# Optimization experiments

Measured on AMD Instinct MI355X. Metric: run time of the kernel, lower is better.

The kernel has to match this reference:

```python
import jax, jax.numpy as jnp
import numpy as np

B, C, H, W = 16, 192, 48, 48
EPS = 1e-5  # torch LayerNorm default


def setup_inputs() -> dict:
    key = jax.random.key(0)
    ks = jax.random.split(key, 5)
    dim = C
    x = jax.random.normal(ks[0], (B, C, H, W), dtype=jnp.float32)
    ln_w = jnp.ones((dim,), dtype=jnp.float32)
    ln_b = jnp.zeros((dim,), dtype=jnp.float32)
    s = 1.0 / np.sqrt(dim)
    Wq = jax.random.uniform(ks[1], (dim, dim), jnp.float32, -s, s)
    Wk = jax.random.uniform(ks[2], (dim, dim), jnp.float32, -s, s)
    Wv = jax.random.uniform(ks[3], (dim, dim), jnp.float32, -s, s)
    w1 = jnp.ones((1,), dtype=jnp.float32)
    w2 = jnp.ones((1,), dtype=jnp.float32)
    return {"x": x, "ln_w": ln_w, "ln_b": ln_b, "Wq": Wq, "Wk": Wk, "Wv": Wv, "w1": w1, "w2": w2}


def reference(x, ln_w, ln_b, Wq, Wk, Wv, w1, w2):
    b, c, h, w = x.shape
    # [B, C, H, W] -> [B, N, C]
    xf = x.reshape(b, c, h * w).transpose(0, 2, 1)
    # LayerNorm over channel dim
    mu = jnp.mean(xf, axis=-1, keepdims=True)
    var = jnp.mean(jnp.square(xf - mu), axis=-1, keepdims=True)
    xn = (xf - mu) * jax.lax.rsqrt(var + EPS) * ln_w + ln_b
    # torch Linear: y = x @ W^T
    Q = jnp.einsum('bnc,dc->bnd', xn, Wq)
    K = jnp.einsum('bnc,dc->bnd', xn, Wk)
    V = jnp.einsum('bnc,dc->bnd', xn, Wv)
    S = jnp.einsum('bnd,bmd->bnm', Q, K)  # [B, N, N]
    attn1 = jax.nn.softmax(S, axis=-1)
    attn2 = jnp.square(jax.nn.relu(S))
    # learned blend weights (softmax over two scalars)
    e1, e2 = jnp.exp(w1), jnp.exp(w2)
    denom = e1 + e2
    attn = (e1 / denom) * attn1 + (e2 / denom) * attn2
    out = jnp.einsum('bnm,bmd->bnd', attn, V)  # [B, N, C]
    out = out.transpose(0, 2, 1).reshape(b, c, h, w)
    return out + x
```

## Files before the change

### kernel.cpp

```cpp
#include <hip/hip_runtime.h>

#define NN 2304
#define CC 192
#define NBATCH 16

typedef unsigned short u16;
typedef __bf16 bf16x8 __attribute__((ext_vector_type(8)));
typedef float f32x4 __attribute__((ext_vector_type(4)));
typedef float f32x16 __attribute__((ext_vector_type(16)));

__device__ __forceinline__ u16 bf16bits(float f) {
  union { float f; unsigned u; } v;
  v.f = f;
  unsigned r = v.u + 0x7FFFu + ((v.u >> 16) & 1u);
  return (u16)(r >> 16);
}

__device__ __forceinline__ uint32_t cvtpk(float lo, float hi) {
  uint32_t d;
  asm("v_cvt_pk_bf16_f32 %0, %1, %2" : "=v"(d) : "v"(lo), "v"(hi));
  return d;
}

__device__ __forceinline__ int swzK(int row, int col) {
  int ch = col >> 3;
  int phys = (ch & ~7) | ((ch ^ row) & 7);
  return row * 192 + (phys << 3) + (col & 7);
}
__device__ __forceinline__ int swz64(int row, int col) {
  int ch = (col >> 3) ^ row;
  return (row << 6) | ((ch & 7) << 3) | (col & 7);
}

__device__ __forceinline__ void gll16(const u16* g, u16* l) {
  __builtin_amdgcn_global_load_lds(
      (const __attribute__((address_space(1))) u16*)g,
      (__attribute__((address_space(3))) u16*)l, 16, 0, 0);
}

__global__ __launch_bounds__(256) void ln_kernel(
    const float* __restrict__ x, const float* __restrict__ lnw,
    const float* __restrict__ lnb, u16* __restrict__ xn) {
  __shared__ float xt[192 * 65];
  __shared__ float psum[4][64], psq[4][64];
  __shared__ float mu_s[64], rs_s[64];
  __shared__ float lw_s[192], lb_s[192];
  int t = threadIdx.x;
  int b = blockIdx.y, n0 = blockIdx.x * 64;
  const float* xb = x + (size_t)b * CC * NN;
  if (t < 192) { lw_s[t] = lnw[t]; lb_s[t] = lnb[t]; }
#pragma unroll
  for (int i = 0; i < 48; ++i) {
    int idx = i * 256 + t;
    int c = idx >> 6, n = idx & 63;
    xt[c * 65 + n] = xb[(size_t)c * NN + n0 + n];
  }
  __syncthreads();
  {
    int n = t & 63, part = t >> 6;
    float s = 0.f, s2 = 0.f;
#pragma unroll
    for (int c = part * 48; c < part * 48 + 48; ++c) {
      float v = xt[c * 65 + n];
      s += v; s2 += v * v;
    }
    psum[part][n] = s; psq[part][n] = s2;
  }
  __syncthreads();
  if (t < 64) {
    float s = psum[0][t] + psum[1][t] + psum[2][t] + psum[3][t];
    float s2 = psq[0][t] + psq[1][t] + psq[2][t] + psq[3][t];
    float mu = s * (1.0f / 192.0f);
    float var = s2 * (1.0f / 192.0f) - mu * mu;
    mu_s[t] = mu;
    rs_s[t] = rsqrtf(var + 1e-5f);
  }
  __syncthreads();
#pragma unroll
  for (int i = 0; i < 12; ++i) {
    int u = i * 256 + t;
    int n = u / 48, cq = (u % 48) * 4;
    float mu = mu_s[n], rs = rs_s[n];
    float v0 = (xt[(cq + 0) * 65 + n] - mu) * rs * lw_s[cq + 0] + lb_s[cq + 0];
    float v1 = (xt[(cq + 1) * 65 + n] - mu) * rs * lw_s[cq + 1] + lb_s[cq + 1];
    float v2 = (xt[(cq + 2) * 65 + n] - mu) * rs * lw_s[cq + 2] + lb_s[cq + 2];
    float v3 = (xt[(cq + 3) * 65 + n] - mu) * rs * lw_s[cq + 3] + lb_s[cq + 3];
    uint2 o;
    o.x = cvtpk(v0, v1);
    o.y = cvtpk(v2, v3);
    *(uint2*)&xn[((size_t)(b * NN + n0 + n)) * CC + cq] = o;
  }
}

__global__ __launch_bounds__(256, 3) void qkv_gemm(
    const u16* __restrict__ xn, const float* __restrict__ Wq,
    const float* __restrict__ Wk, const float* __restrict__ Wv,
    u16* __restrict__ qb, u16* __restrict__ kb, u16* __restrict__ vtb) {
  __shared__ u16 xs[12288];
  __shared__ u16 wsm[12288];
  int t = threadIdx.x, w = t >> 6, lane = t & 63, l15 = lane & 15, qd = lane >> 4;
  int m0 = blockIdx.x * 64, n0 = blockIdx.y * 64, z = blockIdx.z;
  const float* W = (z == 0) ? Wq : (z == 1 ? Wk : Wv);
#pragma unroll
  for (int i = 0; i < 6; ++i) {
    int ch = i * 256 + t;
    int row = ch / 24, cin = (ch % 24) * 8;
    *(uint4*)&xs[swzK(row, cin)] = *(const uint4*)&xn[(size_t)(m0 + row) * 192 + cin];
  }
#pragma unroll
  for (int i = 0; i < 6; ++i) {
    int ch = i * 256 + t;
    int row = ch / 24, cin = (ch % 24) * 8;
    const float* src = &W[(size_t)(n0 + row) * 192 + cin];
    float4 f0 = *(const float4*)src;
    float4 f1 = *(const float4*)(src + 4);
    uint4 o;
    o.x = cvtpk(f0.x, f0.y);
    o.y = cvtpk(f0.z, f0.w);
    o.z = cvtpk(f1.x, f1.y);
    o.w = cvtpk(f1.z, f1.w);
    *(uint4*)&wsm[swzK(row, cin)] = o;
  }
  __syncthreads();
  bf16x8 a[6];
#pragma unroll
  for (int kk = 0; kk < 6; ++kk)
    a[kk] = *(const bf16x8*)&xs[swzK(w * 16 + l15, kk * 32 + qd * 8)];
  const f32x4 fz = {0.f, 0.f, 0.f, 0.f};
  f32x4 acc[4];
#pragma unroll
  for (int ct = 0; ct < 4; ++ct) {
    acc[ct] = fz;
#pragma unroll
    for (int kk = 0; kk < 6; ++kk) {
      bf16x8 bfr = *(const bf16x8*)&wsm[swzK(ct * 16 + l15, kk * 32 + qd * 8)];
      acc[ct] = __builtin_amdgcn_mfma_f32_16x16x32_bf16(a[kk], bfr, acc[ct], 0, 0, 0);
    }
  }
  if (z < 2) {
    u16* outp = (z == 0) ? qb : kb;
#pragma unroll
    for (int ct = 0; ct < 4; ++ct)
#pragma unroll
      for (int r = 0; r < 4; ++r) {
        int m = m0 + w * 16 + qd * 4 + r;
        outp[(size_t)m * 192 + n0 + ct * 16 + l15] = bf16bits(acc[ct][r]);
      }
  } else {
    __syncthreads();
#pragma unroll
    for (int ct = 0; ct < 4; ++ct)
#pragma unroll
      for (int r = 0; r < 4; ++r)
        xs[swz64(ct * 16 + l15, w * 16 + qd * 4 + r)] = bf16bits(acc[ct][r]);
    __syncthreads();
    int b = blockIdx.x / 36, nb = (blockIdx.x % 36) * 64;
#pragma unroll
    for (int i = 0; i < 16; ++i) {
      int idx = i * 256 + t;
      int d = idx >> 6, nn = idx & 63;
      vtb[(size_t)b * 192 * NN + (size_t)(n0 + d) * NN + nb + nn] = xs[swz64(d, nn)];
    }
  }
}

__global__ __launch_bounds__(256, 2) void attn_fused(
    const u16* __restrict__ qb, const u16* __restrict__ kb,
    const u16* __restrict__ vtb, const float* __restrict__ w1p,
    const float* __restrict__ w2p, const float* __restrict__ x,
    float* __restrict__ out) {
  __shared__ u16 sm[32768];
  float* olds = (float*)sm;
  float* lred = (float*)(sm + 24576);

  int t = threadIdx.x, w = t >> 6, lane = t & 63;
  int l31 = lane & 31, hi = lane >> 5;
  int qh = w >> 1, ch = w & 1;
  int bid = blockIdx.x;
  int xcd = bid & 7, j = bid >> 3;
  int b = xcd * 2 + (j >= 36 ? 1 : 0);
  int qt = (j >= 36) ? j - 36 : j;

  const u16* Kg = kb + (size_t)b * NN * CC;
  const u16* Vg = vtb + (size_t)b * CC * NN;
  const u16* Qr = qb + ((size_t)b * NN + qt * 64 + qh * 32 + l31) * CC + hi * 8;
  bf16x8 qf[12];
#pragma unroll
  for (int ks = 0; ks < 12; ++ks) qf[ks] = *(const bf16x8*)(Qr + ks * 16);

  float e1 = __expf(w1p[0]), e2 = __expf(w2p[0]);
  float den = e1 + e2;
  float c1f = e1 / den, c2f = e2 / den;

  u16* pexSW = sm + 24576 + (qh * 2 + ch) * 1024 + lane * 8;
  const u16* pexSR = sm + 24576 + (qh * 2 + (1 - ch)) * 1024 + lane * 8;
  u16* pexRW = sm + 28672 + (qh * 2 + ch) * 1024 + lane * 8;
  const u16* pexRR = sm + 28672 + (qh * 2 + (1 - ch)) * 1024 + lane * 8;

  f32x16 z16;
#pragma unroll
  for (int i = 0; i < 16; ++i) z16[i] = 0.f;
  f32x16 os[3], orl[3];
#pragma unroll
  for (int i = 0; i < 3; ++i) { os[i] = z16; orl[i] = z16; }
  float lsum = 0.f;

#define STAGE_K(KT)                                                        \
  {                                                                        \
    _Pragma("unroll") for (int i = 0; i < 6; ++i) {                        \
      int cid = i * 4 + w, sc = cid * 64 + lane;                           \
      int row = sc / 24, pc = sc % 24;                                     \
      int gc = (pc & ~7) | ((pc ^ row) & 7);                               \
      gll16(Kg + ((size_t)(KT) * 64 + row) * CC + gc * 8, sm + cid * 512); \
    }                                                                      \
  }
#define STAGE_V(KT)                                                        \
  {                                                                        \
    _Pragma("unroll") for (int i = 0; i < 6; ++i) {                        \
      int cid = i * 4 + w, sc = cid * 64 + lane;                           \
      int d = sc >> 3, pc = sc & 7, gc = (pc ^ d) & 7;                     \
      gll16(Vg + (size_t)d * NN + (KT) * 64 + gc * 8,                      \
            sm + 12288 + cid * 512);                                       \
    }                                                                      \
  }

  alignas(16) uint32_t pS0[4], pS1[4], pR0[4], pR1[4];
#define S_BLEND()                                                           \
  {                                                                         \
    f32x16 sA0 = z16, sA1 = z16;                                            \
    __builtin_amdgcn_s_setprio(1);                                          \
    _Pragma("unroll") for (int ks = 0; ks < 6; ++ks) {                      \
      bf16x8 k0 =                                                           \
          *(const bf16x8*)&sm[swzK(ch * 32 + l31, (2 * ks) * 16 + hi * 8)]; \
      bf16x8 k1 =                                                           \
          *(const bf16x8*)&sm[swzK(ch * 32 + l31, (2 * ks + 1) * 16 + hi * 8)]; \
      sA0 = __builtin_amdgcn_mfma_f32_32x32x16_bf16(k0, qf[2 * ks], sA0, 0, 0, 0); \
      sA1 = __builtin_amdgcn_mfma_f32_32x32x16_bf16(k1, qf[2 * ks + 1], sA1, 0, 0, 0); \
    }                                                                       \
    __builtin_amdgcn_s_setprio(0);                                          \
    uint32_t WS[8], WR[8];                                                  \
    _Pragma("unroll") for (int g = 0; g < 4; ++g) {                         \
      float sv0 = sA0[4 * g + 0] + sA1[4 * g + 0];                          \
      float sv1 = sA0[4 * g + 1] + sA1[4 * g + 1];                          \
      float sv2 = sA0[4 * g + 2] + sA1[4 * g + 2];                          \
      float sv3 = sA0[4 * g + 3] + sA1[4 * g + 3];                          \
      float e0 = __expf(fminf(sv0, 60.f));                                  \
      float e1v = __expf(fminf(sv1, 60.f));                                 \
      float e2v = __expf(fminf(sv2, 60.f));                                 \
      float e3 = __expf(fminf(sv3, 60.f));                                  \
      float r0 = fmaxf(sv0, 0.f), r1 = fmaxf(sv1, 0.f);                     \
      float r2 = fmaxf(sv2, 0.f), r3 = fmaxf(sv3, 0.f);                     \
      lsum += (e0 + e1v) + (e2v + e3);                                      \
      WS[2 * g] = cvtpk(e0, e1v);                                           \
      WS[2 * g + 1] = cvtpk(e2v, e3);                                       \
      WR[2 * g] = cvtpk(r0 * r0, r1 * r1);                                  \
      WR[2 * g + 1] = cvtpk(r2 * r2, r3 * r3);                              \
    }                                                                       \
    uint32_t XS[8], XR[8];                                                  \
    _Pragma("unroll") for (int jj = 0; jj < 8; ++jj) {                      \
      XS[jj] = __shfl_xor(WS[jj], 32);                                      \
      XR[jj] = __shfl_xor(WR[jj], 32);                                      \
    }                                                                       \
    pS0[0] = hi ? XS[2] : WS[0]; pS0[1] = hi ? XS[3] : WS[1];               \
    pS0[2] = hi ? WS[2] : XS[0]; pS0[3] = hi ? WS[3] : XS[1];               \
    pS1[0] = hi ? XS[6] : WS[4]; pS1[1] = hi ? XS[7] : WS[5];               \
    pS1[2] = hi ? WS[6] : XS[4]; pS1[3] = hi ? WS[7] : XS[5];               \
    pR0[0] = hi ? XR[2] : WR[0]; pR0[1] = hi ? XR[3] : WR[1];               \
    pR0[2] = hi ? WR[2] : XR[0]; pR0[3] = hi ? WR[3] : XR[1];               \
    pR1[0] = hi ? XR[6] : WR[4]; pR1[1] = hi ? XR[7] : WR[5];               \
    pR1[2] = hi ? WR[6] : XR[4]; pR1[3] = hi ? WR[7] : XR[5];               \
    *(uint4*)pexSW = *(uint4*)pS0;                                          \
    *(uint4*)(pexSW + 512) = *(uint4*)pS1;                                  \
    *(uint4*)pexRW = *(uint4*)pR0;                                          \
    *(uint4*)(pexRW + 512) = *(uint4*)pR1;                                  \
  }

  STAGE_K(0);
  STAGE_V(0);
  asm volatile("s_waitcnt vmcnt(6)\ns_barrier" ::: "memory");
  S_BLEND();
  asm volatile("s_waitcnt lgkmcnt(0)\ns_barrier" ::: "memory");
  STAGE_K(1);

  for (int kt = 0; kt < 36; ++kt) {
    if (kt == 35)
      asm volatile("s_waitcnt vmcnt(0) lgkmcnt(0)\ns_barrier" ::: "memory");
    else
      asm volatile("s_waitcnt vmcnt(6) lgkmcnt(0)\ns_barrier" ::: "memory");

    const u16* vl = sm + 12288;
    uint4 sS0 = *(const uint4*)pexSR;
    uint4 sS1 = *(const uint4*)(pexSR + 512);
    uint4 sR0 = *(const uint4*)pexRR;
    uint4 sR1 = *(const uint4*)(pexRR + 512);
    __builtin_amdgcn_s_setprio(1);
#pragma unroll
    for (int dt = 0; dt < 3; ++dt) {
      int d = ch * 96 + dt * 32 + l31;
      bf16x8 vo0 = *(const bf16x8*)&vl[swz64(d, (ch * 2 + 0) * 16 + hi * 8)];
      bf16x8 vo1 = *(const bf16x8*)&vl[swz64(d, (ch * 2 + 1) * 16 + hi * 8)];
      bf16x8 vs0 = *(const bf16x8*)&vl[swz64(d, ((1 - ch) * 2 + 0) * 16 + hi * 8)];
      bf16x8 vs1 = *(const bf16x8*)&vl[swz64(d, ((1 - ch) * 2 + 1) * 16 + hi * 8)];
      os[dt] = __builtin_amdgcn_mfma_f32_32x32x16_bf16(
          *(const bf16x8*)pS0, vo0, os[dt], 0, 0, 0);
      orl[dt] = __builtin_amdgcn_mfma_f32_32x32x16_bf16(
          *(const bf16x8*)pR0, vo0, orl[dt], 0, 0, 0);
      os[dt] = __builtin_amdgcn_mfma_f32_32x32x16_bf16(
          *(const bf16x8*)pS1, vo1, os[dt], 0, 0, 0);
      orl[dt] = __builtin_amdgcn_mfma_f32_32x32x16_bf16(
          *(const bf16x8*)pR1, vo1, orl[dt], 0, 0, 0);
      os[dt] = __builtin_amdgcn_mfma_f32_32x32x16_bf16(
          *(const bf16x8*)&sS0, vs0, os[dt], 0, 0, 0);
      orl[dt] = __builtin_amdgcn_mfma_f32_32x32x16_bf16(
          *(const bf16x8*)&sR0, vs0, orl[dt], 0, 0, 0);
      os[dt] = __builtin_amdgcn_mfma_f32_32x32x16_bf16(
          *(const bf16x8*)&sS1, vs1, os[dt], 0, 0, 0);
      orl[dt] = __builtin_amdgcn_mfma_f32_32x32x16_bf16(
          *(const bf16x8*)&sR1, vs1, orl[dt], 0, 0, 0);
    }
    __builtin_amdgcn_s_setprio(0);

    if (kt < 35) {
      asm volatile("s_waitcnt vmcnt(0) lgkmcnt(0)\ns_barrier" ::: "memory");
      STAGE_V(kt + 1);
      S_BLEND();
      asm volatile("s_waitcnt lgkmcnt(0)\ns_barrier" ::: "memory");
      if (kt + 2 < 36) STAGE_K(kt + 2);
    }
  }

  lsum += __shfl_xor(lsum, 32);
  __syncthreads();
  if (lane < 32) lred[(qh * 2 + ch) * 32 + l31] = lsum;
  __syncthreads();
  float linv[16];
#pragma unroll
  for (int r = 0; r < 16; ++r) {
    int m = (r & 3) + 8 * (r >> 2) + 4 * hi;
    float ltot = lred[(qh * 2 + 0) * 32 + m] + lred[(qh * 2 + 1) * 32 + m];
    linv[r] = c1f / ltot;
  }
  __syncthreads();
#pragma unroll
  for (int dt = 0; dt < 3; ++dt) {
    int d = ch * 96 + dt * 32 + l31;
#pragma unroll
    for (int r = 0; r < 16; ++r) {
      int m = (r & 3) + 8 * (r >> 2) + 4 * hi;
      int q = qh * 32 + m;
      olds[d * 64 + ((q & ~31) | ((q ^ d) & 31))] =
          os[dt][r] * linv[r] + c2f * orl[dt][r];
    }
  }
  __syncthreads();
  const float* xb = x + (size_t)b * CC * NN + qt * 64;
  float* ob = out + (size_t)b * CC * NN + qt * 64;
#pragma unroll
  for (int i = 0; i < 48; ++i) {
    int idx = i * 256 + t;
    int c = idx >> 6, nn = idx & 63;
    float v = olds[c * 64 + ((nn & ~31) | ((nn ^ c) & 31))];
    ob[(size_t)c * NN + nn] = v + xb[(size_t)c * NN + nn];
  }
#undef STAGE_K
#undef STAGE_V
#undef S_BLEND
}

extern "C" void kernel_launch(void* const* d_in, const int* in_sizes, int n_in,
                              void* d_out, int out_size, void* d_ws, size_t ws_size,
                              hipStream_t stream) {
  (void)in_sizes; (void)n_in; (void)out_size; (void)ws_size;
  const float* x   = (const float*)d_in[0];
  const float* lnw = (const float*)d_in[1];
  const float* lnb = (const float*)d_in[2];
  const float* Wq  = (const float*)d_in[3];
  const float* Wk  = (const float*)d_in[4];
  const float* Wv  = (const float*)d_in[5];
  const float* w1  = (const float*)d_in[6];
  const float* w2  = (const float*)d_in[7];
  float* out = (float*)d_out;

  u16* xn = (u16*)d_ws;
  size_t per = (size_t)NBATCH * NN * CC;
  u16* qb  = xn + per;
  u16* kb  = qb + per;
  u16* vtb = kb + per;

  ln_kernel<<<dim3(36, 16), 256, 0, stream>>>(x, lnw, lnb, xn);
  qkv_gemm<<<dim3(576, 3, 3), 256, 0, stream>>>(xn, Wq, Wk, Wv, qb, kb, vtb);
  attn_fused<<<dim3(576), 256, 0, stream>>>(qb, kb, vtb, w1, w2, x, out);
}
```

Baseline: 283.1 us.

## Pre-convert weights, fuse QKV z-loop, and redo attention key-tile split with V double buffer

A new kernel converts the Q/K/V weights to bf16 once. The QKV GEMM then loads its xn tile a single time and loops over the three projections, prefetching the next weight tile into shared memory with async loads. In the attention kernel, each wave now computes scores for the full 64-key tile itself instead of splitting them across wave pairs and exchanging P through LDS. V is double-buffered and the prologue is simplified. The cost is a redundant QK^T computation per wave pair (double the score MFMAs) and more LDS, in exchange for fewer barriers and less P-exchange traffic.

```diff
diff --git a/kernel.cpp b/kernel.cpp
--- a/kernel.cpp
+++ b/kernel.cpp
@@ -92,74 +92,97 @@
   }
 }
 
+__global__ __launch_bounds__(256) void wconv_kernel(
+    const float* __restrict__ Wq, const float* __restrict__ Wk,
+    const float* __restrict__ Wv, u16* __restrict__ wbf) {
+  int z = blockIdx.y;
+  const float* W = (z == 0) ? Wq : (z == 1 ? Wk : Wv);
+  u16* o = wbf + (size_t)z * 36864;
+  int idx = (blockIdx.x * 256 + (int)threadIdx.x) * 8;
+  float4 f0 = *(const float4*)&W[idx];
+  float4 f1 = *(const float4*)&W[idx + 4];
+  uint4 v;
+  v.x = cvtpk(f0.x, f0.y);
+  v.y = cvtpk(f0.z, f0.w);
+  v.z = cvtpk(f1.x, f1.y);
+  v.w = cvtpk(f1.z, f1.w);
+  *(uint4*)&o[idx] = v;
+}
+
 __global__ __launch_bounds__(256, 3) void qkv_gemm(
-    const u16* __restrict__ xn, const float* __restrict__ Wq,
-    const float* __restrict__ Wk, const float* __restrict__ Wv,
+    const u16* __restrict__ xn, const u16* __restrict__ wbf,
     u16* __restrict__ qb, u16* __restrict__ kb, u16* __restrict__ vtb) {
   __shared__ u16 xs[12288];
   __shared__ u16 wsm[12288];
   int t = threadIdx.x, w = t >> 6, lane = t & 63, l15 = lane & 15, qd = lane >> 4;
-  int m0 = blockIdx.x * 64, n0 = blockIdx.y * 64, z = blockIdx.z;
-  const float* W = (z == 0) ? Wq : (z == 1 ? Wk : Wv);
+  int m0 = blockIdx.x * 64, n0 = blockIdx.y * 64;
+
 #pragma unroll
   for (int i = 0; i < 6; ++i) {
-    int ch = i * 256 + t;
-    int row = ch / 24, cin = (ch % 24) * 8;
-    *(uint4*)&xs[swzK(row, cin)] = *(const uint4*)&xn[(size_t)(m0 + row) * 192 + cin];
+    int cid = i * 4 + w, sc = cid * 64 + lane;
+    int row = sc / 24, pc = sc % 24;
+    int gc = (pc & ~7) | ((pc ^ row) & 7);
+    gll16(xn + (size_t)(m0 + row) * 192 + gc * 8, xs + cid * 512);
   }
 #pragma unroll
   for (int i = 0; i < 6; ++i) {
-    int ch = i * 256 + t;
-    int row = ch / 24, cin = (ch % 24) * 8;
-    const float* src = &W[(size_t)(n0 + row) * 192 + cin];
-    float4 f0 = *(const float4*)src;
-    float4 f1 = *(const float4*)(src + 4);
-    uint4 o;
-    o.x = cvtpk(f0.x, f0.y);
-    o.y = cvtpk(f0.z, f0.w);
-    o.z = cvtpk(f1.x, f1.y);
-    o.w = cvtpk(f1.z, f1.w);
-    *(uint4*)&wsm[swzK(row, cin)] = o;
-  }
-  __syncthreads();
+    int cid = i * 4 + w, sc = cid * 64 + lane;
+    int row = sc / 24, pc = sc % 24;
+    int gc = (pc & ~7) | ((pc ^ row) & 7);
+    gll16(wbf + (size_t)(n0 + row) * 192 + gc * 8, wsm + cid * 512);
+  }
+
   bf16x8 a[6];
-#pragma unroll
-  for (int kk = 0; kk < 6; ++kk)
-    a[kk] = *(const bf16x8*)&xs[swzK(w * 16 + l15, kk * 32 + qd * 8)];
   const f32x4 fz = {0.f, 0.f, 0.f, 0.f};
-  f32x4 acc[4];
-#pragma unroll
-  for (int ct = 0; ct < 4; ++ct) {
-    acc[ct] = fz;
-#pragma unroll
-    for (int kk = 0; kk < 6; ++kk) {
-      bf16x8 bfr = *(const bf16x8*)&wsm[swzK(ct * 16 + l15, kk * 32 + qd * 8)];
-      acc[ct] = __builtin_amdgcn_mfma_f32_16x16x32_bf16(a[kk], bfr, acc[ct], 0, 0, 0);
-    }
-  }
-  if (z < 2) {
-    u16* outp = (z == 0) ? qb : kb;
-#pragma unroll
-    for (int ct = 0; ct < 4; ++ct)
-#pragma unroll
-      for (int r = 0; r < 4; ++r) {
-        int m = m0 + w * 16 + qd * 4 + r;
-        outp[(size_t)m * 192 + n0 + ct * 16 + l15] = bf16bits(acc[ct][r]);
-      }
-  } else {
-    __syncthreads();
-#pragma unroll
-    for (int ct = 0; ct < 4; ++ct)
-#pragma unroll
-      for (int r = 0; r < 4; ++r)
-        xs[swz64(ct * 16 + l15, w * 16 + qd * 4 + r)] = bf16bits(acc[ct][r]);
-    __syncthreads();
-    int b = blockIdx.x / 36, nb = (blockIdx.x % 36) * 64;
-#pragma unroll
-    for (int i = 0; i < 16; ++i) {
-      int idx = i * 256 + t;
-      int d = idx >> 6, nn = idx & 63;
-      vtb[(size_t)b * 192 * NN + (size_t)(n0 + d) * NN + nb + nn] = xs[swz64(d, nn)];
+  for (int z = 0; z < 3; ++z) {
+    asm volatile("s_waitcnt vmcnt(0) lgkmcnt(0)\ns_barrier" ::: "memory");
+    if (z == 0) {
+#pragma unroll
+      for (int kk = 0; kk < 6; ++kk)
+        a[kk] = *(const bf16x8*)&xs[swzK(w * 16 + l15, kk * 32 + qd * 8)];
+    }
+    f32x4 acc[4];
+#pragma unroll
+    for (int ct = 0; ct < 4; ++ct) {
+      acc[ct] = fz;
+#pragma unroll
+      for (int kk = 0; kk < 6; ++kk) {
+        bf16x8 bfr = *(const bf16x8*)&wsm[swzK(ct * 16 + l15, kk * 32 + qd * 8)];
+        acc[ct] = __builtin_amdgcn_mfma_f32_16x16x32_bf16(a[kk], bfr, acc[ct], 0, 0, 0);
+      }
+    }
+    asm volatile("s_waitcnt lgkmcnt(0)\ns_barrier" ::: "memory");
+    if (z < 2) {
+#pragma unroll
+      for (int i = 0; i < 6; ++i) {
+        int cid = i * 4 + w, sc = cid * 64 + lane;
+        int row = sc / 24, pc = sc % 24;
+        int gc = (pc & ~7) | ((pc ^ row) & 7);
+        gll16(wbf + (size_t)(z + 1) * 36864 + (size_t)(n0 + row) * 192 + gc * 8,
+              wsm + cid * 512);
+      }
+      u16* outp = (z == 0) ? qb : kb;
+#pragma unroll
+      for (int ct = 0; ct < 4; ++ct)
+#pragma unroll
+        for (int r = 0; r < 4; ++r) {
+          int m = m0 + w * 16 + qd * 4 + r;
+          outp[(size_t)m * 192 + n0 + ct * 16 + l15] = bf16bits(acc[ct][r]);
+        }
+    } else {
+#pragma unroll
+      for (int ct = 0; ct < 4; ++ct)
+#pragma unroll
+        for (int r = 0; r < 4; ++r)
+          xs[swz64(ct * 16 + l15, w * 16 + qd * 4 + r)] = bf16bits(acc[ct][r]);
+      __syncthreads();
+      int bb = blockIdx.x / 36, nb = (blockIdx.x % 36) * 64;
+#pragma unroll
+      for (int i = 0; i < 16; ++i) {
+        int idx = i * 256 + t;
+        int d = idx >> 6, nn = idx & 63;
+        vtb[(size_t)bb * 192 * NN + (size_t)(n0 + d) * NN + nb + nn] = xs[swz64(d, nn)];
+      }
     }
   }
 }
@@ -169,7 +192,7 @@
     const u16* __restrict__ vtb, const float* __restrict__ w1p,
     const float* __restrict__ w2p, const float* __restrict__ x,
     float* __restrict__ out) {
-  __shared__ u16 sm[32768];
+  __shared__ u16 sm[36864];
   float* olds = (float*)sm;
   float* lred = (float*)(sm + 24576);
 
@@ -191,11 +214,6 @@
   float e1 = __expf(w1p[0]), e2 = __expf(w2p[0]);
   float den = e1 + e2;
   float c1f = e1 / den, c2f = e2 / den;
-
-  u16* pexSW = sm + 24576 + (qh * 2 + ch) * 1024 + lane * 8;
-  const u16* pexSR = sm + 24576 + (qh * 2 + (1 - ch)) * 1024 + lane * 8;
-  u16* pexRW = sm + 28672 + (qh * 2 + ch) * 1024 + lane * 8;
-  const u16* pexRR = sm + 28672 + (qh * 2 + (1 - ch)) * 1024 + lane * 8;
 
   f32x16 z16;
 #pragma unroll
@@ -214,133 +232,102 @@
       gll16(Kg + ((size_t)(KT) * 64 + row) * CC + gc * 8, sm + cid * 512); \
     }                                                                      \
   }
-#define STAGE_V(KT)                                                        \
+#define STAGE_V(KT, BUF)                                                   \
   {                                                                        \
     _Pragma("unroll") for (int i = 0; i < 6; ++i) {                        \
       int cid = i * 4 + w, sc = cid * 64 + lane;                           \
       int d = sc >> 3, pc = sc & 7, gc = (pc ^ d) & 7;                     \
       gll16(Vg + (size_t)d * NN + (KT) * 64 + gc * 8,                      \
-            sm + 12288 + cid * 512);                                       \
+            sm + 12288 + (BUF) * 12288 + cid * 512);                       \
     }                                                                      \
   }
 
-  alignas(16) uint32_t pS0[4], pS1[4], pR0[4], pR1[4];
-#define S_BLEND()                                                           \
-  {                                                                         \
-    f32x16 sA0 = z16, sA1 = z16;                                            \
-    __builtin_amdgcn_s_setprio(1);                                          \
-    _Pragma("unroll") for (int ks = 0; ks < 6; ++ks) {                      \
-      bf16x8 k0 =                                                           \
-          *(const bf16x8*)&sm[swzK(ch * 32 + l31, (2 * ks) * 16 + hi * 8)]; \
-      bf16x8 k1 =                                                           \
-          *(const bf16x8*)&sm[swzK(ch * 32 + l31, (2 * ks + 1) * 16 + hi * 8)]; \
-      sA0 = __builtin_amdgcn_mfma_f32_32x32x16_bf16(k0, qf[2 * ks], sA0, 0, 0, 0); \
-      sA1 = __builtin_amdgcn_mfma_f32_32x32x16_bf16(k1, qf[2 * ks + 1], sA1, 0, 0, 0); \
-    }                                                                       \
-    __builtin_amdgcn_s_setprio(0);                                          \
-    uint32_t WS[8], WR[8];                                                  \
-    _Pragma("unroll") for (int g = 0; g < 4; ++g) {                         \
-      float sv0 = sA0[4 * g + 0] + sA1[4 * g + 0];                          \
-      float sv1 = sA0[4 * g + 1] + sA1[4 * g + 1];                          \
-      float sv2 = sA0[4 * g + 2] + sA1[4 * g + 2];                          \
-      float sv3 = sA0[4 * g + 3] + sA1[4 * g + 3];                          \
-      float e0 = __expf(fminf(sv0, 60.f));                                  \
-      float e1v = __expf(fminf(sv1, 60.f));                                 \
-      float e2v = __expf(fminf(sv2, 60.f));                                 \
-      float e3 = __expf(fminf(sv3, 60.f));                                  \
-      float r0 = fmaxf(sv0, 0.f), r1 = fmaxf(sv1, 0.f);                     \
-      float r2 = fmaxf(sv2, 0.f), r3 = fmaxf(sv3, 0.f);                     \
-      lsum += (e0 + e1v) + (e2v + e3);                                      \
-      WS[2 * g] = cvtpk(e0, e1v);                                           \
-      WS[2 * g + 1] = cvtpk(e2v, e3);                                       \
-      WR[2 * g] = cvtpk(r0 * r0, r1 * r1);                                  \
-      WR[2 * g + 1] = cvtpk(r2 * r2, r3 * r3);                              \
-    }                                                                       \
-    uint32_t XS[8], XR[8];                                                  \
-    _Pragma("unroll") for (int jj = 0; jj < 8; ++jj) {                      \
-      XS[jj] = __shfl_xor(WS[jj], 32);                                      \
-      XR[jj] = __shfl_xor(WR[jj], 32);                                      \
-    }                                                                       \
-    pS0[0] = hi ? XS[2] : WS[0]; pS0[1] = hi ? XS[3] : WS[1];               \
-    pS0[2] = hi ? WS[2] : XS[0]; pS0[3] = hi ? WS[3] : XS[1];               \
-    pS1[0] = hi ? XS[6] : WS[4]; pS1[1] = hi ? XS[7] : WS[5];               \
-    pS1[2] = hi ? WS[6] : XS[4]; pS1[3] = hi ? WS[7] : XS[5];               \
-    pR0[0] = hi ? XR[2] : WR[0]; pR0[1] = hi ? XR[3] : WR[1];               \
-    pR0[2] = hi ? WR[2] : XR[0]; pR0[3] = hi ? WR[3] : XR[1];               \
-    pR1[0] = hi ? XR[6] : WR[4]; pR1[1] = hi ? XR[7] : WR[5];               \
-    pR1[2] = hi ? WR[6] : XR[4]; pR1[3] = hi ? WR[7] : XR[5];               \
-    *(uint4*)pexSW = *(uint4*)pS0;                                          \
-    *(uint4*)(pexSW + 512) = *(uint4*)pS1;                                  \
-    *(uint4*)pexRW = *(uint4*)pR0;                                          \
-    *(uint4*)(pexRW + 512) = *(uint4*)pR1;                                  \
-  }
-
   STAGE_K(0);
-  STAGE_V(0);
-  asm volatile("s_waitcnt vmcnt(6)\ns_barrier" ::: "memory");
-  S_BLEND();
-  asm volatile("s_waitcnt lgkmcnt(0)\ns_barrier" ::: "memory");
-  STAGE_K(1);
+  STAGE_V(0, 0);
+
+  alignas(16) uint32_t pS[4][4], pR[4][4];
 
   for (int kt = 0; kt < 36; ++kt) {
-    if (kt == 35)
-      asm volatile("s_waitcnt vmcnt(0) lgkmcnt(0)\ns_barrier" ::: "memory");
-    else
-      asm volatile("s_waitcnt vmcnt(6) lgkmcnt(0)\ns_barrier" ::: "memory");
-
-    const u16* vl = sm + 12288;
-    uint4 sS0 = *(const uint4*)pexSR;
-    uint4 sS1 = *(const uint4*)(pexSR + 512);
-    uint4 sR0 = *(const uint4*)pexRR;
-    uint4 sR1 = *(const uint4*)(pexRR + 512);
+    asm volatile("s_waitcnt vmcnt(0) lgkmcnt(0)\ns_barrier" ::: "memory");
+    if (kt + 1 < 36) STAGE_V(kt + 1, (kt + 1) & 1);
+
+#pragma unroll
+    for (int kblk = 0; kblk < 2; ++kblk) {
+      f32x16 sA0 = z16, sA1 = z16;
+      __builtin_amdgcn_s_setprio(1);
+#pragma unroll
+      for (int ks = 0; ks < 6; ++ks) {
+        bf16x8 k0 = *(const bf16x8*)&sm[swzK(kblk * 32 + l31, (2 * ks) * 16 + hi * 8)];
+        bf16x8 k1 = *(const bf16x8*)&sm[swzK(kblk * 32 + l31, (2 * ks + 1) * 16 + hi * 8)];
+        sA0 = __builtin_amdgcn_mfma_f32_32x32x16_bf16(k0, qf[2 * ks], sA0, 0, 0, 0);
+        sA1 = __builtin_amdgcn_mfma_f32_32x32x16_bf16(k1, qf[2 * ks + 1], sA1, 0, 0, 0);
+      }
+      __builtin_amdgcn_s_setprio(0);
+      uint32_t WS[8], WR[8];
+#pragma unroll
+      for (int g = 0; g < 4; ++g) {
+        float sv0 = sA0[4 * g + 0] + sA1[4 * g + 0];
+        float sv1 = sA0[4 * g + 1] + sA1[4 * g + 1];
+        float sv2 = sA0[4 * g + 2] + sA1[4 * g + 2];
+        float sv3 = sA0[4 * g + 3] + sA1[4 * g + 3];
+        float ev0 = __expf(fminf(sv0, 60.f));
+        float ev1 = __expf(fminf(sv1, 60.f));
+        float ev2 = __expf(fminf(sv2, 60.f));
+        float ev3 = __expf(fminf(sv3, 60.f));
+        float r0 = fmaxf(sv0, 0.f), r1 = fmaxf(sv1, 0.f);
+        float r2 = fmaxf(sv2, 0.f), r3 = fmaxf(sv3, 0.f);
+        lsum += (ev0 + ev1) + (ev2 + ev3);
+        WS[2 * g] = cvtpk(ev0, ev1);
+        WS[2 * g + 1] = cvtpk(ev2, ev3);
+        WR[2 * g] = cvtpk(r0 * r0, r1 * r1);
+        WR[2 * g + 1] = cvtpk(r2 * r2, r3 * r3);
+      }
+      uint32_t XS[8], XR[8];
+#pragma unroll
+      for (int jj = 0; jj < 8; ++jj) {
+        XS[jj] = __shfl_xor(WS[jj], 32);
+        XR[jj] = __shfl_xor(WR[jj], 32);
+      }
+      pS[2 * kblk][0] = hi ? XS[2] : WS[0]; pS[2 * kblk][1] = hi ? XS[3] : WS[1];
+      pS[2 * kblk][2] = hi ? WS[2] : XS[0]; pS[2 * kblk][3] = hi ? WS[3] : XS[1];
+      pS[2 * kblk + 1][0] = hi ? XS[6] : WS[4]; pS[2 * kblk + 1][1] = hi ? XS[7] : WS[5];
+      pS[2 * kblk + 1][2] = hi ? WS[6] : XS[4]; pS[2 * kblk + 1][3] = hi ? WS[7] : XS[5];
+      pR[2 * kblk][0] = hi ? XR[2] : WR[0]; pR[2 * kblk][1] = hi ? XR[3] : WR[1];
+      pR[2 * kblk][2] = hi ? WR[2] : XR[0]; pR[2 * kblk][3] = hi ? WR[3] : XR[1];
+      pR[2 * kblk + 1][0] = hi ? XR[6] : WR[4]; pR[2 * kblk + 1][1] = hi ? XR[7] : WR[5];
+      pR[2 * kblk + 1][2] = hi ? WR[6] : XR[4]; pR[2 * kblk + 1][3] = hi ? WR[7] : XR[5];
+    }
+
+    asm volatile("s_waitcnt lgkmcnt(0)\ns_barrier" ::: "memory");
+    if (kt + 1 < 36) STAGE_K(kt + 1);
+
+    const u16* vl = sm + 12288 + (kt & 1) * 12288;
     __builtin_amdgcn_s_setprio(1);
 #pragma unroll
     for (int dt = 0; dt < 3; ++dt) {
       int d = ch * 96 + dt * 32 + l31;
-      bf16x8 vo0 = *(const bf16x8*)&vl[swz64(d, (ch * 2 + 0) * 16 + hi * 8)];
-      bf16x8 vo1 = *(const bf16x8*)&vl[swz64(d, (ch * 2 + 1) * 16 + hi * 8)];
-      bf16x8 vs0 = *(const bf16x8*)&vl[swz64(d, ((1 - ch) * 2 + 0) * 16 + hi * 8)];
-      bf16x8 vs1 = *(const bf16x8*)&vl[swz64(d, ((1 - ch) * 2 + 1) * 16 + hi * 8)];
-      os[dt] = __builtin_amdgcn_mfma_f32_32x32x16_bf16(
-          *(const bf16x8*)pS0, vo0, os[dt], 0, 0, 0);
-      orl[dt] = __builtin_amdgcn_mfma_f32_32x32x16_bf16(
-          *(const bf16x8*)pR0, vo0, orl[dt], 0, 0, 0);
-      os[dt] = __builtin_amdgcn_mfma_f32_32x32x16_bf16(
-          *(const bf16x8*)pS1, vo1, os[dt], 0, 0, 0);
-      orl[dt] = __builtin_amdgcn_mfma_f32_32x32x16_bf16(
-          *(const bf16x8*)pR1, vo1, orl[dt], 0, 0, 0);
-      os[dt] = __builtin_amdgcn_mfma_f32_32x32x16_bf16(
-          *(const bf16x8*)&sS0, vs0, os[dt], 0, 0, 0);
-      orl[dt] = __builtin_amdgcn_mfma_f32_32x32x16_bf16(
-          *(const bf16x8*)&sR0, vs0, orl[dt], 0, 0, 0);
-      os[dt] = __builtin_amdgcn_mfma_f32_32x32x16_bf16(
-          *(const bf16x8*)&sS1, vs1, os[dt], 0, 0, 0);
-      orl[dt] = __builtin_amdgcn_mfma_f32_32x32x16_bf16(
-          *(const bf16x8*)&sR1, vs1, orl[dt], 0, 0, 0);
+#pragma unroll
+      for (int ks = 0; ks < 4; ++ks) {
+        bf16x8 vf = *(const bf16x8*)&vl[swz64(d, ks * 16 + hi * 8)];
+        os[dt] = __builtin_amdgcn_mfma_f32_32x32x16_bf16(
+            *(const bf16x8*)pS[ks], vf, os[dt], 0, 0, 0);
+        orl[dt] = __builtin_amdgcn_mfma_f32_32x32x16_bf16(
+            *(const bf16x8*)pR[ks], vf, orl[dt], 0, 0, 0);
+      }
     }
     __builtin_amdgcn_s_setprio(0);
-
-    if (kt < 35) {
-      asm volatile("s_waitcnt vmcnt(0) lgkmcnt(0)\ns_barrier" ::: "memory");
-      STAGE_V(kt + 1);
-      S_BLEND();
-      asm volatile("s_waitcnt lgkmcnt(0)\ns_barrier" ::: "memory");
-      if (kt + 2 < 36) STAGE_K(kt + 2);
-    }
   }
 
   lsum += __shfl_xor(lsum, 32);
   __syncthreads();
-  if (lane < 32) lred[(qh * 2 + ch) * 32 + l31] = lsum;
+  if (ch == 0 && hi == 0) lred[qh * 32 + l31] = lsum;
   __syncthreads();
   float linv[16];
 #pragma unroll
   for (int r = 0; r < 16; ++r) {
     int m = (r & 3) + 8 * (r >> 2) + 4 * hi;
-    float ltot = lred[(qh * 2 + 0) * 32 + m] + lred[(qh * 2 + 1) * 32 + m];
-    linv[r] = c1f / ltot;
-  }
-  __syncthreads();
+    linv[r] = c1f / lred[qh * 32 + m];
+  }
 #pragma unroll
   for (int dt = 0; dt < 3; ++dt) {
     int d = ch * 96 + dt * 32 + l31;
@@ -364,7 +351,6 @@
   }
 #undef STAGE_K
 #undef STAGE_V
-#undef S_BLEND
 }
 
 extern "C" void kernel_launch(void* const* d_in, const int* in_sizes, int n_in,
@@ -386,8 +372,10 @@
   u16* qb  = xn + per;
   u16* kb  = qb + per;
   u16* vtb = kb + per;
+  u16* wbf = vtb + per;
 
   ln_kernel<<<dim3(36, 16), 256, 0, stream>>>(x, lnw, lnb, xn);
-  qkv_gemm<<<dim3(576, 3, 3), 256, 0, stream>>>(xn, Wq, Wk, Wv, qb, kb, vtb);
+  wconv_kernel<<<dim3(18, 3), 256, 0, stream>>>(Wq, Wk, Wv, wbf);
+  qkv_gemm<<<dim3(576, 3), 256, 0, stream>>>(xn, wbf, qb, kb, vtb);
   attn_fused<<<dim3(576), 256, 0, stream>>>(qb, kb, vtb, w1, w2, x, out);
 }
```

Result: slower. 608.7 us (+115.0%).
